# Kernel optimization log

Hardware: AMD Instinct MI355X
Metric: run time of the kernel (lower is better)

Reference implementation:

```python
import jax, jax.numpy as jnp
import numpy as np

RES = 192      # resolution
RANK = 8       # low-rank
FD = 32        # feature_dim
NFPD = 32      # num_features_per_dim = round(32768**(1/3))
RADIUS = 1.3
NI = 128       # n_intersections
STEP = 0.0352  # step_size
B = 2048       # rays


def setup_inputs():
    key = jax.random.key(0)
    ks = jax.random.split(key, 12)
    ro = jax.random.normal(ks[0], (B, 3), dtype=jnp.float32)
    ro = ro / jnp.linalg.norm(ro, axis=-1, keepdims=True) * 2.5  # origins outside the cube
    rd = -ro + 0.1 * jax.random.normal(ks[1], (B, 3), dtype=jnp.float32)
    rd = rd / jnp.linalg.norm(rd, axis=-1, keepdims=True)        # roughly toward origin
    def nrm(k, shape, std):
        return std * jax.random.normal(k, shape, dtype=jnp.float32)
    return {
        "rays_o": ro, "rays_d": rd,
        "Gxy": nrm(ks[2], (RES, RES, 3, RANK), 0.1),
        "Gxz": nrm(ks[3], (RES, RES, 3, RANK), 0.1),
        "Gyz": nrm(ks[4], (RES, RES, 3, RANK), 0.1),
        "F_grid": nrm(ks[5], (NFPD, NFPD, NFPD, FD), 0.05),
        "sW0": nrm(ks[6], (FD, 128), FD ** -0.5),
        "sW1": nrm(ks[7], (128, 128), 128 ** -0.5),
        "sW2": nrm(ks[8], (128, 16), 128 ** -0.5),
        "cW0": nrm(ks[9], (31, 64), 31 ** -0.5),
        "cW1": nrm(ks[10], (64, 64), 64 ** -0.5),
        "cW2": nrm(ks[11], (64, 3), 64 ** -0.5),
    }


def trilinear(vol, coords):
    # vol: [D,H,W,C]; coords: [N,3] as (x,y,z) in [-1,1]; x indexes W (last spatial dim)
    # matches torch grid_sample(align_corners=True, mode='bilinear', padding_mode='border')
    D, H, W, C = vol.shape
    def prep(c, size):
        idx = jnp.clip((c + 1.0) * 0.5 * (size - 1), 0.0, size - 1.0)  # border clamp
        i0 = jnp.clip(jnp.floor(idx).astype(jnp.int32), 0, size - 2)
        return i0, i0 + 1, idx - i0
    x0, x1, wx = prep(coords[:, 0], W)
    y0, y1, wy = prep(coords[:, 1], H)
    z0, z1, wz = prep(coords[:, 2], D)
    wx = wx[:, None]; wy = wy[:, None]; wz = wz[:, None]
    def g(zi, yi, xi):
        return vol[zi, yi, xi]  # [N,C]
    c00 = g(z0, y0, x0) * (1 - wx) + g(z0, y0, x1) * wx
    c01 = g(z0, y1, x0) * (1 - wx) + g(z0, y1, x1) * wx
    c10 = g(z1, y0, x0) * (1 - wx) + g(z1, y0, x1) * wx
    c11 = g(z1, y1, x0) * (1 - wx) + g(z1, y1, x1) * wx
    c0 = c00 * (1 - wy) + c01 * wy
    c1 = c10 * (1 - wy) + c11 * wy
    return c0 * (1 - wz) + c1 * wz


def sh16(d):
    # tcnn SphericalHarmonics degree 4 on directions (input (d+1)/2 is unmapped back to d internally)
    x, y, z = d[:, 0], d[:, 1], d[:, 2]
    x2, y2, z2 = x * x, y * y, z * z
    return jnp.stack([
        jnp.full_like(x, 0.28209479177387814),
        -0.48860251190291987 * y,
        0.48860251190291987 * z,
        -0.48860251190291987 * x,
        1.0925484305920792 * x * y,
        -1.0925484305920792 * y * z,
        0.94617469575755997 * z2 - 0.31539156525251999,
        -1.0925484305920792 * x * z,
        0.54627421529603959 * (x2 - y2),
        0.59004358992664352 * y * (-3.0 * x2 + y2),
        2.8906114426405538 * x * y * z,
        0.45704579946446572 * y * (1.0 - 5.0 * z2),
        0.3731763325901154 * z * (5.0 * z2 - 3.0),
        0.45704579946446572 * x * (1.0 - 5.0 * z2),
        1.445305721320277 * z * (x2 - y2),
        0.59004358992664352 * x * (-x2 + 3.0 * y2),
    ], axis=-1)


def _forward(rays_o, rays_d, Gxy, Gxz, Gyz, F_grid, sW0, sW1, sW2, cW0, cW1, cW2):
    b = rays_o.shape[0]
    # --- get_intersections: ray/AABB [-R,R]^3, uniform marching ---
    d = jnp.where(jnp.abs(rays_d) < 1e-9, 1e-9, rays_d)
    t1 = (-RADIUS - rays_o) / d
    t2 = (RADIUS - rays_o) / d
    tmin = jnp.max(jnp.minimum(t1, t2), axis=-1)
    tmax = jnp.min(jnp.maximum(t1, t2), axis=-1)
    near = jnp.maximum(tmin, 0.0)
    ts = near[:, None] + jnp.arange(NI + 1, dtype=jnp.float32) * STEP  # intersections [B,NI+1]
    tmid = 0.5 * (ts[:, :-1] + ts[:, 1:])                              # [B,NI]
    pts = rays_o[:, None, :] + tmid[..., None] * rays_d[:, None, :]    # [B,NI,3]
    mask = (jnp.all(jnp.abs(pts) <= RADIUS, axis=-1)
            & (tmid <= tmax[:, None]) & (tmax > tmin)[:, None])        # [B,NI]
    rdn = rays_d / jnp.linalg.norm(rays_d, axis=-1, keepdims=True)
    # coordinate chain of forward + eval_pts nets out to pts/RADIUS in [-1,1]
    p = ((pts / RADIUS + 1.0) * RES / 2.0) * 2.0 / RES - 1.0
    pf = p.reshape(-1, 3)
    # --- densify low-rank tri-plane grid: sum_r Gxy*Gxz*Gyz -> [RES,RES,RES,3] ---
    grid = jnp.zeros((RES, RES, RES, 3), dtype=Gxy.dtype)
    for r in range(RANK):  # fixed small rank; avoids a [RES^3,3,RANK] intermediate
        grid = grid + (Gxy[:, :, None, :, r] * Gxz[:, None, :, :, r] * Gyz[None, :, :, :, r])
    # --- eval_pts: grid_sample -> hash-feature grid_sample -> MLPs ---
    Gvals = trilinear(grid, pf)            # [N,3]
    Fvals = trilinear(F_grid, Gvals)       # [N,FD]
    h = jax.nn.relu(Fvals @ sW0)
    h = jax.nn.relu(h @ sW1)
    out16 = h @ sW2                        # [N,16]
    sigma = out16[:, 0].reshape(b, NI)
    sigma = jax.nn.relu(jnp.where(mask, sigma, 0.0))
    rdn_pts = jnp.broadcast_to(rdn[:, None, :], (b, NI, 3)).reshape(-1, 3)
    ci = jnp.concatenate([sh16(rdn_pts), out16[:, 1:]], axis=-1)  # [N,31]
    c = jax.nn.relu(ci @ cW0)
    c = jax.nn.relu(c @ cW1)
    color = (c @ cW2).reshape(b, NI, 3)
    color = jnp.where(mask[..., None], color, 0.0)
    # --- sigma2alpha + shrgb2rgb (white background) ---
    dists = ts[:, 1:] - ts[:, :-1]         # |rdn| == 1
    alpha = 1.0 - jnp.exp(-sigma * dists)
    T = jnp.cumprod(1.0 - alpha + 1e-10, axis=-1)
    T = jnp.concatenate([jnp.ones_like(T[:, :1]), T[:, :-1]], axis=-1)  # exclusive
    w = alpha * T                          # abs_light [B,NI]
    rgb = jax.nn.sigmoid(color)
    acc = jnp.sum(w, axis=-1)
    return jnp.sum(w[..., None] * rgb, axis=1) + (1.0 - acc)[..., None]  # [B,3]


def reference(rays_o, rays_d, Gxy, Gxz, Gyz, F_grid, sW0, sW1, sW2, cW0, cW1, cW2):
    return _forward(rays_o, rays_d, Gxy, Gxz, Gyz, F_grid, sW0, sW1, sW2, cW0, cW1, cW2)
```

## Files before the change

### kernel.cpp

```cpp
#include <hip/hip_runtime.h>
#include <math.h>

#define RES 192
#define RANK 8
#define NI 128
#define LW 136

typedef __attribute__((ext_vector_type(8))) short short8;
typedef __attribute__((ext_vector_type(4))) float floatx4;

#define OFF_SW0 0
#define OFF_SW1 4096
#define OFF_SW2 20480
#define OFF_CW0 22528
#define OFF_CW1 24576
#define OFF_CW2 28672
#define PACK_TOTAL 29696

#define TRI_CELLS (RES*RES)
#define TRI_TOTAL (3*TRI_CELLS*24)
#define FG_TOTAL  (32*32*32*32)
#define PREP_TOTAL (PACK_TOTAL + TRI_TOTAL + FG_TOTAL)

__device__ __forceinline__ short f2bf(float x){
    unsigned u = __float_as_uint(x);
    unsigned r = (u + 0x7FFFu + ((u >> 16) & 1u)) >> 16;
    return (short)r;
}
__device__ __forceinline__ float bf2f(short s){
    return __uint_as_float(((unsigned)(unsigned short)s) << 16);
}

__device__ __forceinline__ void prep_idx(float c, int size, int& i0, float& f){
    float idx = (c + 1.0f)*0.5f*(float)(size-1);
    idx = fminf(fmaxf(idx, 0.0f), (float)(size-1));
    int ii = (int)idx;
    if (ii > size-2) ii = size-2;
    i0 = ii;
    f = idx - (float)ii;
}

__device__ __forceinline__ float wred64(float v){
    #pragma unroll
    for (int o=32;o>0;o>>=1) v += __shfl_down(v, o, 64);
    return v;
}

__global__ void __launch_bounds__(256) prep_all(
    const float* __restrict__ sW0, const float* __restrict__ sW1,
    const float* __restrict__ sW2, const float* __restrict__ cW0,
    const float* __restrict__ cW1, const float* __restrict__ cW2,
    const float* __restrict__ Gxy, const float* __restrict__ Gxz,
    const float* __restrict__ Gyz, const float* __restrict__ F_grid,
    short* __restrict__ Wp, short* __restrict__ Gp, short* __restrict__ Fg)
{
    int e = blockIdx.x*256 + threadIdx.x;
    if (e < PACK_TOTAL){
        const float* src; int K, N, ksteps, base;
        if      (e < OFF_SW1){ src=sW0; K=32;  N=128; ksteps=1; base=OFF_SW0; }
        else if (e < OFF_SW2){ src=sW1; K=128; N=128; ksteps=4; base=OFF_SW1; }
        else if (e < OFF_CW0){ src=sW2; K=128; N=16;  ksteps=4; base=OFF_SW2; }
        else if (e < OFF_CW1){ src=cW0; K=31;  N=64;  ksteps=1; base=OFF_CW0; }
        else if (e < OFF_CW2){ src=cW1; K=64;  N=64;  ksteps=2; base=OFF_CW1; }
        else                 { src=cW2; K=64;  N=3;   ksteps=2; base=OFF_CW2; }
        int i = e - base;
        int j = i & 7, lane = (i>>3)&63, t = i>>9;
        int ks = t % ksteps, nt = t / ksteps;
        int k = ks*32 + (lane>>4)*8 + j;
        int n = nt*16 + (lane&15);
        float v = (k < K && n < N) ? src[k*N + n] : 0.0f;
        Wp[e] = f2bf(v);
        return;
    }
    int e2 = e - PACK_TOTAL;
    if (e2 < TRI_TOTAL){
        int p    = e2 / (TRI_CELLS*24);
        int rem  = e2 - p*(TRI_CELLS*24);
        int cell = rem / 24;
        int c    = rem - cell*24;
        const float* src = (p==0) ? Gxy : (p==1) ? Gxz : Gyz;
        Gp[((size_t)(p*TRI_CELLS + cell))*32 + c] = f2bf(src[(size_t)cell*24 + c]);
        return;
    }
    int e3 = e2 - TRI_TOTAL;
    Fg[e3] = f2bf(F_grid[e3]);
}

__global__ void __launch_bounds__(256) interp2(
    const float* __restrict__ rays_o, const float* __restrict__ rays_d,
    const short* __restrict__ Gp, const short* __restrict__ Fg,
    short* __restrict__ FvOut)
{
    const int tid = threadIdx.x;
    const int ray = blockIdx.x;
    const int s   = tid >> 1;
    const int h   = tid & 1;

    const float ox = rays_o[ray*3+0], oy = rays_o[ray*3+1], oz = rays_o[ray*3+2];
    const float dx = rays_d[ray*3+0], dy = rays_d[ray*3+1], dz = rays_d[ray*3+2];

    float sdx = (fabsf(dx) < 1e-9f) ? 1e-9f : dx;
    float sdy = (fabsf(dy) < 1e-9f) ? 1e-9f : dy;
    float sdz = (fabsf(dz) < 1e-9f) ? 1e-9f : dz;
    float t1x = (-1.3f - ox)/sdx, t2x = (1.3f - ox)/sdx;
    float t1y = (-1.3f - oy)/sdy, t2y = (1.3f - oy)/sdy;
    float t1z = (-1.3f - oz)/sdz, t2z = (1.3f - oz)/sdz;
    float tmin = fmaxf(fminf(t1x,t2x), fmaxf(fminf(t1y,t2y), fminf(t1z,t2z)));
    float tmax = fminf(fmaxf(t1x,t2x), fminf(fmaxf(t1y,t2y), fmaxf(t1z,t2z)));
    float nearv = fmaxf(tmin, 0.0f);

    float ts0 = nearv + (float)s     * 0.0352f;
    float ts1 = nearv + (float)(s+1) * 0.0352f;
    float tmid = 0.5f*(ts0+ts1);
    float px = ox + tmid*dx, py = oy + tmid*dy, pz = oz + tmid*dz;
    bool mask = (fabsf(px)<=1.3f) && (fabsf(py)<=1.3f) && (fabsf(pz)<=1.3f)
              && (tmid<=tmax) && (tmax>tmin);

    short8 o0 = {0,0,0,0,0,0,0,0};
    short8 o1 = {0,0,0,0,0,0,0,0};

    if (mask){
        float p0 = (px/1.3f + 1.0f)*192.0f/2.0f*2.0f/192.0f - 1.0f;
        float p1 = (py/1.3f + 1.0f)*192.0f/2.0f*2.0f/192.0f - 1.0f;
        float p2 = (pz/1.3f + 1.0f)*192.0f/2.0f*2.0f/192.0f - 1.0f;

        int x0, y0, z0; float fx, fy, fz;
        prep_idx(p0, RES, x0, fx);
        prep_idx(p1, RES, y0, fy);
        prep_idx(p2, RES, z0, fz);

        const int zi = z0 + h;
        const float wzc = h ? fz : (1.0f - fz);

        short8 XY[2][3], XZ[2][3], YZ[2][2][3];
        {
            const short8* pxy0 = (const short8*)(Gp + ((size_t)(zi*RES + y0  ))*32);
            const short8* pxy1 = (const short8*)(Gp + ((size_t)(zi*RES + y0+1))*32);
            const short8* pxz0 = (const short8*)(Gp + ((size_t)(TRI_CELLS + zi*RES + x0  ))*32);
            const short8* pxz1 = (const short8*)(Gp + ((size_t)(TRI_CELLS + zi*RES + x0+1))*32);
            const short8* pyz00 = (const short8*)(Gp + ((size_t)(2*TRI_CELLS + (y0  )*RES + x0  ))*32);
            const short8* pyz01 = (const short8*)(Gp + ((size_t)(2*TRI_CELLS + (y0  )*RES + x0+1))*32);
            const short8* pyz10 = (const short8*)(Gp + ((size_t)(2*TRI_CELLS + (y0+1)*RES + x0  ))*32);
            const short8* pyz11 = (const short8*)(Gp + ((size_t)(2*TRI_CELLS + (y0+1)*RES + x0+1))*32);
            #pragma unroll
            for (int q=0;q<3;q++){
                XY[0][q]=pxy0[q]; XY[1][q]=pxy1[q];
                XZ[0][q]=pxz0[q]; XZ[1][q]=pxz1[q];
                YZ[0][0][q]=pyz00[q]; YZ[0][1][q]=pyz01[q];
                YZ[1][0][q]=pyz10[q]; YZ[1][1][q]=pyz11[q];
            }
        }

        float gv0=0.f, gv1=0.f, gv2=0.f;
        #pragma unroll
        for (int yc=0; yc<2; yc++){
            const float wy = yc ? fy : (1.0f - fy);
            #pragma unroll
            for (int xc=0; xc<2; xc++){
                const float wx = xc ? fx : (1.0f - fx);
                const float w = wzc*wy*wx;
                float s0=0.f, s1=0.f, s2=0.f;
                #pragma unroll
                for (int r=0;r<8;r++){
                    s0 = fmaf(bf2f(XY[yc][0][r])*bf2f(XZ[xc][0][r]), bf2f(YZ[yc][xc][0][r]), s0);
                    s1 = fmaf(bf2f(XY[yc][1][r])*bf2f(XZ[xc][1][r]), bf2f(YZ[yc][xc][1][r]), s1);
                    s2 = fmaf(bf2f(XY[yc][2][r])*bf2f(XZ[xc][2][r]), bf2f(YZ[yc][xc][2][r]), s2);
                }
                gv0 = fmaf(w, s0, gv0);
                gv1 = fmaf(w, s1, gv1);
                gv2 = fmaf(w, s2, gv2);
            }
        }
        gv0 += __shfl_xor(gv0, 1, 64);
        gv1 += __shfl_xor(gv1, 1, 64);
        gv2 += __shfl_xor(gv2, 1, 64);

        int a0,b0,c0; float fa,fb,fc;
        prep_idx(gv2, 32, a0, fa);
        prep_idx(gv1, 32, b0, fb);
        prep_idx(gv0, 32, c0, fc);
        float Fv[16];
        #pragma unroll
        for (int k=0;k<16;k++) Fv[k]=0.f;
        #pragma unroll
        for (int zc=0; zc<2; zc++){
            const int zi2 = a0+zc; const float wz2 = zc ? fa : 1.f-fa;
            #pragma unroll
            for (int yc=0; yc<2; yc++){
                const int yi2 = b0+yc; const float wy2 = yc ? fb : 1.f-fb;
                #pragma unroll
                for (int xc=0; xc<2; xc++){
                    const int xi2 = c0+xc; const float wx2 = xc ? fc : 1.f-fc;
                    const float w = wz2*wy2*wx2;
                    const short8* pf = (const short8*)(Fg + ((size_t)((zi2*32+yi2)*32+xi2))*32 + h*16);
                    short8 v0 = pf[0], v1 = pf[1];
                    #pragma unroll
                    for (int j=0;j<8;j++){
                        Fv[j]   = fmaf(w, bf2f(v0[j]), Fv[j]);
                        Fv[8+j] = fmaf(w, bf2f(v1[j]), Fv[8+j]);
                    }
                }
            }
        }
        #pragma unroll
        for (int j=0;j<8;j++){ o0[j] = f2bf(Fv[j]); o1[j] = f2bf(Fv[8+j]); }
    }

    short* dstp = FvOut + (((size_t)ray*128 + s)*32 + h*16);
    *(short8*)dstp       = o0;
    *(short8*)(dstp + 8) = o1;
}

__launch_bounds__(256, 4)
__global__ void nerf_mlp(
    const float* __restrict__ rays_o, const float* __restrict__ rays_d,
    const short* __restrict__ Wp, const short* __restrict__ Fv,
    float* __restrict__ out)
{
    __shared__ short buf[128*LW];
    __shared__ float sigmaArr[128];
    __shared__ float rgbArr[128*3];
    __shared__ float wtot[2];
    __shared__ float partial[8];

    const int tid  = threadIdx.x;
    const int lane = tid & 63;
    const int wv   = tid >> 6;
    const int ray  = blockIdx.x;

    const float ox = rays_o[ray*3+0], oy = rays_o[ray*3+1], oz = rays_o[ray*3+2];
    const float dx = rays_d[ray*3+0], dy = rays_d[ray*3+1], dz = rays_d[ray*3+2];

    float sdx = (fabsf(dx) < 1e-9f) ? 1e-9f : dx;
    float sdy = (fabsf(dy) < 1e-9f) ? 1e-9f : dy;
    float sdz = (fabsf(dz) < 1e-9f) ? 1e-9f : dz;
    float t1x = (-1.3f - ox)/sdx, t2x = (1.3f - ox)/sdx;
    float t1y = (-1.3f - oy)/sdy, t2y = (1.3f - oy)/sdy;
    float t1z = (-1.3f - oz)/sdz, t2z = (1.3f - oz)/sdz;
    float tmin = fmaxf(fminf(t1x,t2x), fmaxf(fminf(t1y,t2y), fminf(t1z,t2z)));
    float tmax = fminf(fmaxf(t1x,t2x), fminf(fmaxf(t1y,t2y), fmaxf(t1z,t2z)));
    float nearv = fmaxf(tmin, 0.0f);

    const int rowbase = wv*32;
    const int col  = lane & 15;
    const int quad = lane >> 4;
    const int ar0  = rowbase + col;
    const int ar1  = ar0 + 16;

    {
        int sid = rowbase + (lane & 31);
        float w_ts0 = nearv + (float)sid     * 0.0352f;
        float w_ts1 = nearv + (float)(sid+1) * 0.0352f;
        float w_tm  = 0.5f*(w_ts0+w_ts1);
        float wpx = ox + w_tm*dx, wpy = oy + w_tm*dy, wpz = oz + w_tm*dz;
        bool m = (fabsf(wpx)<=1.3f) && (fabsf(wpy)<=1.3f) && (fabsf(wpz)<=1.3f)
               && (w_tm<=tmax) && (tmax>tmin);
        if (__ballot(m) == 0ULL) goto composite;
    }

    {
        const short8* FvG = (const short8*)(Fv + (size_t)ray*128*32);
        short8 a0 = FvG[ar0*4 + quad];
        short8 a1 = FvG[ar1*4 + quad];
        const short8* W = (const short8*)(Wp + OFF_SW0);
        #pragma unroll
        for (int nt=0; nt<8; nt++){
            short8 b = W[nt*64 + lane];
            floatx4 c0v = {0.f,0.f,0.f,0.f}, c1v = {0.f,0.f,0.f,0.f};
            c0v = __builtin_amdgcn_mfma_f32_16x16x32_bf16(a0, b, c0v, 0,0,0);
            c1v = __builtin_amdgcn_mfma_f32_16x16x32_bf16(a1, b, c1v, 0,0,0);
            #pragma unroll
            for (int r=0;r<4;r++){
                int row0 = rowbase + quad*4 + r;
                buf[row0*LW      + nt*16 + col] = f2bf(fmaxf(c0v[r],0.f));
                buf[(row0+16)*LW + nt*16 + col] = f2bf(fmaxf(c1v[r],0.f));
            }
        }
    }

    {
        short8 A0[4], A1[4];
        #pragma unroll
        for (int ks=0;ks<4;ks++){
            A0[ks] = *(const short8*)&buf[ar0*LW + ks*32 + quad*8];
            A1[ks] = *(const short8*)&buf[ar1*LW + ks*32 + quad*8];
        }
        const short8* W = (const short8*)(Wp + OFF_SW1);
        #pragma unroll
        for (int nt=0; nt<8; nt++){
            floatx4 c0v = {0.f,0.f,0.f,0.f}, c1v = {0.f,0.f,0.f,0.f};
            #pragma unroll
            for (int ks=0;ks<4;ks++){
                short8 b = W[(nt*4+ks)*64 + lane];
                c0v = __builtin_amdgcn_mfma_f32_16x16x32_bf16(A0[ks], b, c0v, 0,0,0);
                c1v = __builtin_amdgcn_mfma_f32_16x16x32_bf16(A1[ks], b, c1v, 0,0,0);
            }
            #pragma unroll
            for (int r=0;r<4;r++){
                int row0 = rowbase + quad*4 + r;
                buf[row0*LW      + nt*16 + col] = f2bf(fmaxf(c0v[r],0.f));
                buf[(row0+16)*LW + nt*16 + col] = f2bf(fmaxf(c1v[r],0.f));
            }
        }
    }

    {
        short8 A0[4], A1[4];
        #pragma unroll
        for (int ks=0;ks<4;ks++){
            A0[ks] = *(const short8*)&buf[ar0*LW + ks*32 + quad*8];
            A1[ks] = *(const short8*)&buf[ar1*LW + ks*32 + quad*8];
        }
        const short8* W = (const short8*)(Wp + OFF_SW2);
        floatx4 c0v = {0.f,0.f,0.f,0.f}, c1v = {0.f,0.f,0.f,0.f};
        #pragma unroll
        for (int ks=0;ks<4;ks++){
            short8 b = W[ks*64 + lane];
            c0v = __builtin_amdgcn_mfma_f32_16x16x32_bf16(A0[ks], b, c0v, 0,0,0);
            c1v = __builtin_amdgcn_mfma_f32_16x16x32_bf16(A1[ks], b, c1v, 0,0,0);
        }
        #pragma unroll
        for (int r=0;r<4;r++){
            int row0 = rowbase + quad*4 + r;
            if (col == 0){
                sigmaArr[row0]    = c0v[r];
                sigmaArr[row0+16] = c1v[r];
            } else {
                buf[row0*LW      + 15 + col] = f2bf(c0v[r]);
                buf[(row0+16)*LW + 15 + col] = f2bf(c1v[r]);
            }
        }
        const float dn = sqrtf(dx*dx+dy*dy+dz*dz);
        const float X = dx/dn, Y = dy/dn, Z = dz/dn;
        const float X2=X*X, Y2=Y*Y, Z2=Z*Z;
        float sh[16];
        sh[0]= 0.28209479177387814f;
        sh[1]=-0.48860251190291987f*Y;
        sh[2]= 0.48860251190291987f*Z;
        sh[3]=-0.48860251190291987f*X;
        sh[4]= 1.0925484305920792f*X*Y;
        sh[5]=-1.0925484305920792f*Y*Z;
        sh[6]= 0.94617469575756f*Z2 - 0.31539156525252f;
        sh[7]=-1.0925484305920792f*X*Z;
        sh[8]= 0.5462742152960396f*(X2-Y2);
        sh[9]= 0.5900435899266435f*Y*(-3.0f*X2+Y2);
        sh[10]=2.890611442640554f*X*Y*Z;
        sh[11]=0.4570457994644657f*Y*(1.0f-5.0f*Z2);
        sh[12]=0.3731763325901154f*Z*(5.0f*Z2-3.0f);
        sh[13]=0.4570457994644657f*X*(1.0f-5.0f*Z2);
        sh[14]=1.445305721320277f*Z*(X2-Y2);
        sh[15]=0.5900435899266435f*X*(-X2+3.0f*Y2);
        if (lane < 32){
            int row = rowbase + lane;
            #pragma unroll
            for (int k=0;k<16;k++) buf[row*LW + k] = f2bf(sh[k]);
        }
    }

    {
        short8 a0 = *(const short8*)&buf[ar0*LW + quad*8];
        short8 a1 = *(const short8*)&buf[ar1*LW + quad*8];
        const short8* W = (const short8*)(Wp + OFF_CW0);
        #pragma unroll
        for (int nt=0; nt<4; nt++){
            short8 b = W[nt*64 + lane];
            floatx4 c0v = {0.f,0.f,0.f,0.f}, c1v = {0.f,0.f,0.f,0.f};
            c0v = __builtin_amdgcn_mfma_f32_16x16x32_bf16(a0, b, c0v, 0,0,0);
            c1v = __builtin_amdgcn_mfma_f32_16x16x32_bf16(a1, b, c1v, 0,0,0);
            #pragma unroll
            for (int r=0;r<4;r++){
                int row0 = rowbase + quad*4 + r;
                buf[row0*LW      + nt*16 + col] = f2bf(fmaxf(c0v[r],0.f));
                buf[(row0+16)*LW + nt*16 + col] = f2bf(fmaxf(c1v[r],0.f));
            }
        }
    }

    {
        short8 A0[2], A1[2];
        #pragma unroll
        for (int ks=0;ks<2;ks++){
            A0[ks] = *(const short8*)&buf[ar0*LW + ks*32 + quad*8];
            A1[ks] = *(const short8*)&buf[ar1*LW + ks*32 + quad*8];
        }
        const short8* W = (const short8*)(Wp + OFF_CW1);
        #pragma unroll
        for (int nt=0; nt<4; nt++){
            floatx4 c0v = {0.f,0.f,0.f,0.f}, c1v = {0.f,0.f,0.f,0.f};
            #pragma unroll
            for (int ks=0;ks<2;ks++){
                short8 b = W[(nt*2+ks)*64 + lane];
                c0v = __builtin_amdgcn_mfma_f32_16x16x32_bf16(A0[ks], b, c0v, 0,0,0);
                c1v = __builtin_amdgcn_mfma_f32_16x16x32_bf16(A1[ks], b, c1v, 0,0,0);
            }
            #pragma unroll
            for (int r=0;r<4;r++){
                int row0 = rowbase + quad*4 + r;
                buf[row0*LW      + nt*16 + col] = f2bf(fmaxf(c0v[r],0.f));
                buf[(row0+16)*LW + nt*16 + col] = f2bf(fmaxf(c1v[r],0.f));
            }
        }
    }

    {
        short8 A0[2], A1[2];
        #pragma unroll
        for (int ks=0;ks<2;ks++){
            A0[ks] = *(const short8*)&buf[ar0*LW + ks*32 + quad*8];
            A1[ks] = *(const short8*)&buf[ar1*LW + ks*32 + quad*8];
        }
        const short8* W = (const short8*)(Wp + OFF_CW2);
        floatx4 c0v = {0.f,0.f,0.f,0.f}, c1v = {0.f,0.f,0.f,0.f};
        #pragma unroll
        for (int ks=0;ks<2;ks++){
            short8 b = W[ks*64 + lane];
            c0v = __builtin_amdgcn_mfma_f32_16x16x32_bf16(A0[ks], b, c0v, 0,0,0);
            c1v = __builtin_amdgcn_mfma_f32_16x16x32_bf16(A1[ks], b, c1v, 0,0,0);
        }
        if (col < 3){
            #pragma unroll
            for (int r=0;r<4;r++){
                int row0 = rowbase + quad*4 + r;
                rgbArr[row0*3 + col]      = c0v[r];
                rgbArr[(row0+16)*3 + col] = c1v[r];
            }
        }
    }

composite:
    __syncthreads();

    {
        float alpha = 0.f, rr = 0.f, rg = 0.f, rb = 0.f;
        if (tid < 128){
            float ts0 = nearv + (float)tid     * 0.0352f;
            float ts1 = nearv + (float)(tid+1) * 0.0352f;
            float tmid = 0.5f*(ts0+ts1);
            float dist = ts1 - ts0;
            float px = ox + tmid*dx, py = oy + tmid*dy, pz = oz + tmid*dz;
            bool mask = (fabsf(px)<=1.3f) && (fabsf(py)<=1.3f) && (fabsf(pz)<=1.3f)
                      && (tmid<=tmax) && (tmax>tmin);
            float sg = mask ? fmaxf(sigmaArr[tid], 0.f) : 0.f;
            alpha = 1.0f - expf(-sg*dist);
            if (mask){
                rr = 1.0f/(1.0f+expf(-rgbArr[tid*3+0]));
                rg = 1.0f/(1.0f+expf(-rgbArr[tid*3+1]));
                rb = 1.0f/(1.0f+expf(-rgbArr[tid*3+2]));
            }
        }
        float p = 1.0f - alpha + 1e-10f;
        #pragma unroll
        for (int off=1; off<64; off<<=1){
            float u = __shfl_up(p, off, 64);
            if (lane >= off) p *= u;
        }
        if (tid < 128 && lane == 63) wtot[wv] = p;
        float excl = __shfl_up(p, 1, 64);
        if (lane == 0) excl = 1.0f;
        __syncthreads();
        if (tid < 128){
            float T = excl;
            if (wv == 1) T *= wtot[0];
            float w = alpha * T;
            float v0 = wred64(w*rr);
            float v1 = wred64(w*rg);
            float v2 = wred64(w*rb);
            float v3 = wred64(w);
            if (lane == 0){
                partial[wv*4+0]=v0; partial[wv*4+1]=v1; partial[wv*4+2]=v2; partial[wv*4+3]=v3;
            }
        }
        __syncthreads();
        if (tid == 0){
            float acc = partial[3] + partial[7];
            float bg  = 1.0f - acc;
            out[ray*3+0] = partial[0] + partial[4] + bg;
            out[ray*3+1] = partial[1] + partial[5] + bg;
            out[ray*3+2] = partial[2] + partial[6] + bg;
        }
    }
}

extern "C" void kernel_launch(void* const* d_in, const int* in_sizes, int n_in,
                              void* d_out, int out_size, void* d_ws, size_t ws_size,
                              hipStream_t stream){
    const float* rays_o = (const float*)d_in[0];
    const float* rays_d = (const float*)d_in[1];
    const float* Gxy    = (const float*)d_in[2];
    const float* Gxz    = (const float*)d_in[3];
    const float* Gyz    = (const float*)d_in[4];
    const float* F_grid = (const float*)d_in[5];
    const float* sW0    = (const float*)d_in[6];
    const float* sW1    = (const float*)d_in[7];
    const float* sW2    = (const float*)d_in[8];
    const float* cW0    = (const float*)d_in[9];
    const float* cW1    = (const float*)d_in[10];
    const float* cW2    = (const float*)d_in[11];

    short* Wp   = (short*)d_ws;
    short* FvWS = Wp   + PACK_TOTAL;
    short* Gp   = FvWS + (size_t)2048*128*32;
    short* Fg   = Gp   + (size_t)3*TRI_CELLS*32;

    prep_all<<<PREP_TOTAL/256, 256, 0, stream>>>(sW0,sW1,sW2,cW0,cW1,cW2,
                                                 Gxy,Gxz,Gyz,F_grid, Wp,Gp,Fg);
    interp2<<<2048, 256, 0, stream>>>(rays_o, rays_d, Gp, Fg, FvWS);
    nerf_mlp<<<2048, 256, 0, stream>>>(rays_o, rays_d, Wp, FvWS, (float*)d_out);
}
```

Measured before the change: 144.4 us.

## Fuse interpolation kernel into MLP kernel via shared-memory feature staging

Merges the feature interpolation kernel into the MLP/compositing kernel. Each wave now computes the interpolated features for its own 32 samples and writes them to LDS, and the first MFMA layer reads them from there. This removes the global workspace round trip of the per-sample features and one kernel launch. In exchange, the fused kernel carries more register pressure under launch_bounds(256,4), and rays where the whole wave is masked skip the interpolation entirely.

```diff
diff --git a/kernel.cpp b/kernel.cpp
--- a/kernel.cpp
+++ b/kernel.cpp
@@ -86,15 +86,22 @@
     Fg[e3] = f2bf(F_grid[e3]);
 }
 
-__global__ void __launch_bounds__(256) interp2(
+__launch_bounds__(256, 4)
+__global__ void nerf_fused(
     const float* __restrict__ rays_o, const float* __restrict__ rays_d,
     const short* __restrict__ Gp, const short* __restrict__ Fg,
-    short* __restrict__ FvOut)
+    const short* __restrict__ Wp, float* __restrict__ out)
 {
-    const int tid = threadIdx.x;
-    const int ray = blockIdx.x;
-    const int s   = tid >> 1;
-    const int h   = tid & 1;
+    __shared__ short buf[128*LW];
+    __shared__ float sigmaArr[128];
+    __shared__ float rgbArr[128*3];
+    __shared__ float wtot[2];
+    __shared__ float partial[8];
+
+    const int tid  = threadIdx.x;
+    const int lane = tid & 63;
+    const int wv   = tid >> 6;
+    const int ray  = blockIdx.x;
 
     const float ox = rays_o[ray*3+0], oy = rays_o[ray*3+1], oz = rays_o[ray*3+2];
     const float dx = rays_d[ray*3+0], dy = rays_d[ray*3+1], dz = rays_d[ray*3+2];
@@ -109,138 +116,6 @@
     float tmax = fminf(fmaxf(t1x,t2x), fminf(fmaxf(t1y,t2y), fmaxf(t1z,t2z)));
     float nearv = fmaxf(tmin, 0.0f);
 
-    float ts0 = nearv + (float)s     * 0.0352f;
-    float ts1 = nearv + (float)(s+1) * 0.0352f;
-    float tmid = 0.5f*(ts0+ts1);
-    float px = ox + tmid*dx, py = oy + tmid*dy, pz = oz + tmid*dz;
-    bool mask = (fabsf(px)<=1.3f) && (fabsf(py)<=1.3f) && (fabsf(pz)<=1.3f)
-              && (tmid<=tmax) && (tmax>tmin);
-
-    short8 o0 = {0,0,0,0,0,0,0,0};
-    short8 o1 = {0,0,0,0,0,0,0,0};
-
-    if (mask){
-        float p0 = (px/1.3f + 1.0f)*192.0f/2.0f*2.0f/192.0f - 1.0f;
-        float p1 = (py/1.3f + 1.0f)*192.0f/2.0f*2.0f/192.0f - 1.0f;
-        float p2 = (pz/1.3f + 1.0f)*192.0f/2.0f*2.0f/192.0f - 1.0f;
-
-        int x0, y0, z0; float fx, fy, fz;
-        prep_idx(p0, RES, x0, fx);
-        prep_idx(p1, RES, y0, fy);
-        prep_idx(p2, RES, z0, fz);
-
-        const int zi = z0 + h;
-        const float wzc = h ? fz : (1.0f - fz);
-
-        short8 XY[2][3], XZ[2][3], YZ[2][2][3];
-        {
-            const short8* pxy0 = (const short8*)(Gp + ((size_t)(zi*RES + y0  ))*32);
-            const short8* pxy1 = (const short8*)(Gp + ((size_t)(zi*RES + y0+1))*32);
-            const short8* pxz0 = (const short8*)(Gp + ((size_t)(TRI_CELLS + zi*RES + x0  ))*32);
-            const short8* pxz1 = (const short8*)(Gp + ((size_t)(TRI_CELLS + zi*RES + x0+1))*32);
-            const short8* pyz00 = (const short8*)(Gp + ((size_t)(2*TRI_CELLS + (y0  )*RES + x0  ))*32);
-            const short8* pyz01 = (const short8*)(Gp + ((size_t)(2*TRI_CELLS + (y0  )*RES + x0+1))*32);
-            const short8* pyz10 = (const short8*)(Gp + ((size_t)(2*TRI_CELLS + (y0+1)*RES + x0  ))*32);
-            const short8* pyz11 = (const short8*)(Gp + ((size_t)(2*TRI_CELLS + (y0+1)*RES + x0+1))*32);
-            #pragma unroll
-            for (int q=0;q<3;q++){
-                XY[0][q]=pxy0[q]; XY[1][q]=pxy1[q];
-                XZ[0][q]=pxz0[q]; XZ[1][q]=pxz1[q];
-                YZ[0][0][q]=pyz00[q]; YZ[0][1][q]=pyz01[q];
-                YZ[1][0][q]=pyz10[q]; YZ[1][1][q]=pyz11[q];
-            }
-        }
-
-        float gv0=0.f, gv1=0.f, gv2=0.f;
-        #pragma unroll
-        for (int yc=0; yc<2; yc++){
-            const float wy = yc ? fy : (1.0f - fy);
-            #pragma unroll
-            for (int xc=0; xc<2; xc++){
-                const float wx = xc ? fx : (1.0f - fx);
-                const float w = wzc*wy*wx;
-                float s0=0.f, s1=0.f, s2=0.f;
-                #pragma unroll
-                for (int r=0;r<8;r++){
-                    s0 = fmaf(bf2f(XY[yc][0][r])*bf2f(XZ[xc][0][r]), bf2f(YZ[yc][xc][0][r]), s0);
-                    s1 = fmaf(bf2f(XY[yc][1][r])*bf2f(XZ[xc][1][r]), bf2f(YZ[yc][xc][1][r]), s1);
-                    s2 = fmaf(bf2f(XY[yc][2][r])*bf2f(XZ[xc][2][r]), bf2f(YZ[yc][xc][2][r]), s2);
-                }
-                gv0 = fmaf(w, s0, gv0);
-                gv1 = fmaf(w, s1, gv1);
-                gv2 = fmaf(w, s2, gv2);
-            }
-        }
-        gv0 += __shfl_xor(gv0, 1, 64);
-        gv1 += __shfl_xor(gv1, 1, 64);
-        gv2 += __shfl_xor(gv2, 1, 64);
-
-        int a0,b0,c0; float fa,fb,fc;
-        prep_idx(gv2, 32, a0, fa);
-        prep_idx(gv1, 32, b0, fb);
-        prep_idx(gv0, 32, c0, fc);
-        float Fv[16];
-        #pragma unroll
-        for (int k=0;k<16;k++) Fv[k]=0.f;
-        #pragma unroll
-        for (int zc=0; zc<2; zc++){
-            const int zi2 = a0+zc; const float wz2 = zc ? fa : 1.f-fa;
-            #pragma unroll
-            for (int yc=0; yc<2; yc++){
-                const int yi2 = b0+yc; const float wy2 = yc ? fb : 1.f-fb;
-                #pragma unroll
-                for (int xc=0; xc<2; xc++){
-                    const int xi2 = c0+xc; const float wx2 = xc ? fc : 1.f-fc;
-                    const float w = wz2*wy2*wx2;
-                    const short8* pf = (const short8*)(Fg + ((size_t)((zi2*32+yi2)*32+xi2))*32 + h*16);
-                    short8 v0 = pf[0], v1 = pf[1];
-                    #pragma unroll
-                    for (int j=0;j<8;j++){
-                        Fv[j]   = fmaf(w, bf2f(v0[j]), Fv[j]);
-                        Fv[8+j] = fmaf(w, bf2f(v1[j]), Fv[8+j]);
-                    }
-                }
-            }
-        }
-        #pragma unroll
-        for (int j=0;j<8;j++){ o0[j] = f2bf(Fv[j]); o1[j] = f2bf(Fv[8+j]); }
-    }
-
-    short* dstp = FvOut + (((size_t)ray*128 + s)*32 + h*16);
-    *(short8*)dstp       = o0;
-    *(short8*)(dstp + 8) = o1;
-}
-
-__launch_bounds__(256, 4)
-__global__ void nerf_mlp(
-    const float* __restrict__ rays_o, const float* __restrict__ rays_d,
-    const short* __restrict__ Wp, const short* __restrict__ Fv,
-    float* __restrict__ out)
-{
-    __shared__ short buf[128*LW];
-    __shared__ float sigmaArr[128];
-    __shared__ float rgbArr[128*3];
-    __shared__ float wtot[2];
-    __shared__ float partial[8];
-
-    const int tid  = threadIdx.x;
-    const int lane = tid & 63;
-    const int wv   = tid >> 6;
-    const int ray  = blockIdx.x;
-
-    const float ox = rays_o[ray*3+0], oy = rays_o[ray*3+1], oz = rays_o[ray*3+2];
-    const float dx = rays_d[ray*3+0], dy = rays_d[ray*3+1], dz = rays_d[ray*3+2];
-
-    float sdx = (fabsf(dx) < 1e-9f) ? 1e-9f : dx;
-    float sdy = (fabsf(dy) < 1e-9f) ? 1e-9f : dy;
-    float sdz = (fabsf(dz) < 1e-9f) ? 1e-9f : dz;
-    float t1x = (-1.3f - ox)/sdx, t2x = (1.3f - ox)/sdx;
-    float t1y = (-1.3f - oy)/sdy, t2y = (1.3f - oy)/sdy;
-    float t1z = (-1.3f - oz)/sdz, t2z = (1.3f - oz)/sdz;
-    float tmin = fmaxf(fminf(t1x,t2x), fmaxf(fminf(t1y,t2y), fminf(t1z,t2z)));
-    float tmax = fminf(fmaxf(t1x,t2x), fminf(fmaxf(t1y,t2y), fmaxf(t1z,t2z)));
-    float nearv = fmaxf(tmin, 0.0f);
-
     const int rowbase = wv*32;
     const int col  = lane & 15;
     const int quad = lane >> 4;
@@ -259,9 +134,113 @@
     }
 
     {
-        const short8* FvG = (const short8*)(Fv + (size_t)ray*128*32);
-        short8 a0 = FvG[ar0*4 + quad];
-        short8 a1 = FvG[ar1*4 + quad];
+        const int s = rowbase + (lane >> 1);
+        const int h = lane & 1;
+
+        float ts0 = nearv + (float)s     * 0.0352f;
+        float ts1 = nearv + (float)(s+1) * 0.0352f;
+        float tmid = 0.5f*(ts0+ts1);
+        float px = ox + tmid*dx, py = oy + tmid*dy, pz = oz + tmid*dz;
+        bool mask = (fabsf(px)<=1.3f) && (fabsf(py)<=1.3f) && (fabsf(pz)<=1.3f)
+                  && (tmid<=tmax) && (tmax>tmin);
+
+        short8 o0 = {0,0,0,0,0,0,0,0};
+        short8 o1 = {0,0,0,0,0,0,0,0};
+
+        if (mask){
+            float p0 = (px/1.3f + 1.0f)*192.0f/2.0f*2.0f/192.0f - 1.0f;
+            float p1 = (py/1.3f + 1.0f)*192.0f/2.0f*2.0f/192.0f - 1.0f;
+            float p2 = (pz/1.3f + 1.0f)*192.0f/2.0f*2.0f/192.0f - 1.0f;
+
+            int x0, y0, z0; float fx, fy, fz;
+            prep_idx(p0, RES, x0, fx);
+            prep_idx(p1, RES, y0, fy);
+            prep_idx(p2, RES, z0, fz);
+
+            const int zi = z0 + h;
+            const float wzc = h ? fz : (1.0f - fz);
+
+            short8 XY[2][3], XZ[2][3], YZ[2][2][3];
+            {
+                const short8* pxy0 = (const short8*)(Gp + ((size_t)(zi*RES + y0  ))*32);
+                const short8* pxy1 = (const short8*)(Gp + ((size_t)(zi*RES + y0+1))*32);
+                const short8* pxz0 = (const short8*)(Gp + ((size_t)(TRI_CELLS + zi*RES + x0  ))*32);
+                const short8* pxz1 = (const short8*)(Gp + ((size_t)(TRI_CELLS + zi*RES + x0+1))*32);
+                const short8* pyz00 = (const short8*)(Gp + ((size_t)(2*TRI_CELLS + (y0  )*RES + x0  ))*32);
+                const short8* pyz01 = (const short8*)(Gp + ((size_t)(2*TRI_CELLS + (y0  )*RES + x0+1))*32);
+                const short8* pyz10 = (const short8*)(Gp + ((size_t)(2*TRI_CELLS + (y0+1)*RES + x0  ))*32);
+                const short8* pyz11 = (const short8*)(Gp + ((size_t)(2*TRI_CELLS + (y0+1)*RES + x0+1))*32);
+                #pragma unroll
+                for (int q=0;q<3;q++){
+                    XY[0][q]=pxy0[q]; XY[1][q]=pxy1[q];
+                    XZ[0][q]=pxz0[q]; XZ[1][q]=pxz1[q];
+                    YZ[0][0][q]=pyz00[q]; YZ[0][1][q]=pyz01[q];
+                    YZ[1][0][q]=pyz10[q]; YZ[1][1][q]=pyz11[q];
+                }
+            }
+
+            float gv0=0.f, gv1=0.f, gv2=0.f;
+            #pragma unroll
+            for (int yc=0; yc<2; yc++){
+                const float wy = yc ? fy : (1.0f - fy);
+                #pragma unroll
+                for (int xc=0; xc<2; xc++){
+                    const float wx = xc ? fx : (1.0f - fx);
+                    const float w = wzc*wy*wx;
+                    float q0=0.f, q1=0.f, q2=0.f;
+                    #pragma unroll
+                    for (int r=0;r<8;r++){
+                        q0 = fmaf(bf2f(XY[yc][0][r])*bf2f(XZ[xc][0][r]), bf2f(YZ[yc][xc][0][r]), q0);
+                        q1 = fmaf(bf2f(XY[yc][1][r])*bf2f(XZ[xc][1][r]), bf2f(YZ[yc][xc][1][r]), q1);
+                        q2 = fmaf(bf2f(XY[yc][2][r])*bf2f(XZ[xc][2][r]), bf2f(YZ[yc][xc][2][r]), q2);
+                    }
+                    gv0 = fmaf(w, q0, gv0);
+                    gv1 = fmaf(w, q1, gv1);
+                    gv2 = fmaf(w, q2, gv2);
+                }
+            }
+            gv0 += __shfl_xor(gv0, 1, 64);
+            gv1 += __shfl_xor(gv1, 1, 64);
+            gv2 += __shfl_xor(gv2, 1, 64);
+
+            int a0,b0,c0; float fa,fb,fc;
+            prep_idx(gv2, 32, a0, fa);
+            prep_idx(gv1, 32, b0, fb);
+            prep_idx(gv0, 32, c0, fc);
+            float Fv[16];
+            #pragma unroll
+            for (int k=0;k<16;k++) Fv[k]=0.f;
+            #pragma unroll
+            for (int zc=0; zc<2; zc++){
+                const int zi2 = a0+zc; const float wz2 = zc ? fa : 1.f-fa;
+                #pragma unroll
+                for (int yc=0; yc<2; yc++){
+                    const int yi2 = b0+yc; const float wy2 = yc ? fb : 1.f-fb;
+                    #pragma unroll
+                    for (int xc=0; xc<2; xc++){
+                        const int xi2 = c0+xc; const float wx2 = xc ? fc : 1.f-fc;
+                        const float w = wz2*wy2*wx2;
+                        const short8* pf = (const short8*)(Fg + ((size_t)((zi2*32+yi2)*32+xi2))*32 + h*16);
+                        short8 v0 = pf[0], v1 = pf[1];
+                        #pragma unroll
+                        for (int j=0;j<8;j++){
+                            Fv[j]   = fmaf(w, bf2f(v0[j]), Fv[j]);
+                            Fv[8+j] = fmaf(w, bf2f(v1[j]), Fv[8+j]);
+                        }
+                    }
+                }
+            }
+            #pragma unroll
+            for (int j=0;j<8;j++){ o0[j] = f2bf(Fv[j]); o1[j] = f2bf(Fv[8+j]); }
+        }
+
+        *(short8*)&buf[s*LW + h*16]     = o0;
+        *(short8*)&buf[s*LW + h*16 + 8] = o1;
+    }
+
+    {
+        short8 a0 = *(const short8*)&buf[ar0*LW + quad*8];
+        short8 a1 = *(const short8*)&buf[ar1*LW + quad*8];
         const short8* W = (const short8*)(Wp + OFF_SW0);
         #pragma unroll
         for (int nt=0; nt<8; nt++){
@@ -497,13 +476,11 @@
     const float* cW1    = (const float*)d_in[10];
     const float* cW2    = (const float*)d_in[11];
 
-    short* Wp   = (short*)d_ws;
-    short* FvWS = Wp   + PACK_TOTAL;
-    short* Gp   = FvWS + (size_t)2048*128*32;
-    short* Fg   = Gp   + (size_t)3*TRI_CELLS*32;
+    short* Wp = (short*)d_ws;
+    short* Gp = Wp + PACK_TOTAL;
+    short* Fg = Gp + (size_t)3*TRI_CELLS*32;
 
     prep_all<<<PREP_TOTAL/256, 256, 0, stream>>>(sW0,sW1,sW2,cW0,cW1,cW2,
                                                  Gxy,Gxz,Gyz,F_grid, Wp,Gp,Fg);
-    interp2<<<2048, 256, 0, stream>>>(rays_o, rays_d, Gp, Fg, FvWS);
-    nerf_mlp<<<2048, 256, 0, stream>>>(rays_o, rays_d, Wp, FvWS, (float*)d_out);
-}
+    nerf_fused<<<2048, 256, 0, stream>>>(rays_o, rays_d, Gp, Fg, Wp, (float*)d_out);
+}
```

Measured after the change: 136.7 us. 1.06x faster.
